# Kernel optimization log

Measured on AMD Instinct MI355X. Metric: run time of the kernel, lower is better.

Reference implementation:

```python
import jax, jax.numpy as jnp
import numpy as np

N = 100000
E = 1600000
C = 192      # in_channels
GH = 256     # grapher hidden
FH = 512     # ffn hidden
EPS = 1e-5


def _bn(x, gamma, beta):
    # BatchNorm1d, training-mode batch statistics over the node axis
    mean = jnp.mean(x, axis=0)
    var = jnp.var(x, axis=0)
    return (x - mean) * jax.lax.rsqrt(var + EPS) * gamma + beta


def setup_inputs() -> dict:
    key = jax.random.key(0)
    ks = jax.random.split(key, 12)
    s = 0.02
    inp = {
        "x": jax.random.normal(ks[0], (N, C), dtype=jnp.float32),
        "edge_index": jax.random.randint(ks[1], (2, E), 0, N, dtype=jnp.int64),
        # Grapher fc1
        "Wg1": jax.random.normal(ks[2], (C, GH), jnp.float32) * s,
        "bg1": jnp.zeros((GH,), jnp.float32),
        "gg1": jnp.ones((GH,), jnp.float32),
        "beg1": jnp.zeros((GH,), jnp.float32),
        # GraphConv (lin_rel has bias, lin_root no bias, per PyG)
        "Wrel": jax.random.normal(ks[3], (GH, GH), jnp.float32) * s,
        "brel": jnp.zeros((GH,), jnp.float32),
        "Wroot": jax.random.normal(ks[4], (GH, GH), jnp.float32) * s,
        # Grapher fc2
        "Wg2": jax.random.normal(ks[5], (GH, C), jnp.float32) * s,
        "bg2": jnp.zeros((C,), jnp.float32),
        "gg2": jnp.ones((C,), jnp.float32),
        "beg2": jnp.zeros((C,), jnp.float32),
        # FFN fc1
        "Wf1": jax.random.normal(ks[6], (C, FH), jnp.float32) * s,
        "bf1": jnp.zeros((FH,), jnp.float32),
        "gf1": jnp.ones((FH,), jnp.float32),
        "bef1": jnp.zeros((FH,), jnp.float32),
        # FFN fc2
        "Wf2": jax.random.normal(ks[7], (FH, C), jnp.float32) * s,
        "bf2": jnp.zeros((C,), jnp.float32),
        "gf2": jnp.ones((C,), jnp.float32),
        "bef2": jnp.zeros((C,), jnp.float32),
    }
    return inp


def reference(x, edge_index, Wg1, bg1, gg1, beg1, Wrel, brel, Wroot,
              Wg2, bg2, gg2, beg2, Wf1, bf1, gf1, bef1, Wf2, bf2, gf2, bef2):
    n = x.shape[0]
    src, dst = edge_index[0], edge_index[1]

    # ---- Grapher ----
    shortcut = x
    h = _bn(x @ Wg1 + bg1, gg1, beg1)                       # [N, GH]
    # GraphConv: sum-aggregate neighbor messages at target nodes
    agg = jax.ops.segment_sum(h[src], dst, num_segments=n)  # [N, GH]
    gc = agg @ Wrel + brel + h @ Wroot
    h = jax.nn.gelu(gc, approximate=False)
    h = _bn(h @ Wg2 + bg2, gg2, beg2)                       # [N, C]
    x = h + shortcut

    # ---- FFN ----
    shortcut = x
    h = jax.nn.gelu(_bn(x @ Wf1 + bf1, gf1, bef1), approximate=False)
    h = _bn(h @ Wf2 + bf2, gf2, bef2)
    return h + shortcut
```

## Files before the change

kernel.cpp:

```cpp
#include <hip/hip_runtime.h>
#include <math.h>

typedef __bf16 bf16x8 __attribute__((ext_vector_type(8)));
typedef float  floatx4 __attribute__((ext_vector_type(4)));

__device__ inline float bf_lo(unsigned u){ return __uint_as_float(u << 16); }
__device__ inline float bf_hi(unsigned u){ return __uint_as_float(u & 0xffff0000u); }
__device__ inline unsigned short f2bf_u(float f){
    unsigned u = __float_as_uint(f);
    return (unsigned short)((u + 0x7fffu + ((u >> 16) & 1u)) >> 16);
}
__device__ inline unsigned pack2(float a, float b){
    return (unsigned)f2bf_u(a) | ((unsigned)f2bf_u(b) << 16);
}
__device__ inline float gelu_f(float v){
    return 0.5f * v * (1.f + erff(v * 0.70710678118654752f));
}
__device__ inline void gload_lds16(const void* g, void* l){
    __builtin_amdgcn_global_load_lds(
        (const __attribute__((address_space(1))) unsigned int*)g,
        (__attribute__((address_space(3))) unsigned int*)l, 16, 0, 0);
}

__global__ void zero_k(int* __restrict__ p, int n){
    int i = blockIdx.x * 256 + threadIdx.x;
    if (i < n) p[i] = 0;
}

__global__ void xcast_k(const float* __restrict__ x, unsigned short* __restrict__ xb, long n8){
    long i = (long)blockIdx.x * 256 + threadIdx.x;
    if (i < n8){
        const float4* p = (const float4*)(x + i * 8);
        float4 a = p[0], b = p[1];
        uint4 o;
        o.x = pack2(a.x, a.y); o.y = pack2(a.z, a.w);
        o.z = pack2(b.x, b.y); o.w = pack2(b.z, b.w);
        *(uint4*)(xb + i * 8) = o;
    }
}

__global__ void wprep_k(const float* __restrict__ W, unsigned short* __restrict__ Wt,
                        int K, int Ncols, int ostride, int ooffs){
    int idx = blockIdx.x * 256 + threadIdx.x;
    if (idx < K * Ncols){
        int k = idx / Ncols, n = idx - k * Ncols;
        Wt[(size_t)n * ostride + ooffs + k] = f2bf_u(W[idx]);
    }
}


#define RBSH 9
#define RB   512
#define PCH  8192

__global__ __launch_bounds__(256)
void bhist_k(const int* __restrict__ dst, int* __restrict__ bcnt, int E){
    __shared__ int h[256];
    for (int i = threadIdx.x; i < 256; i += 256) h[i] = 0;
    __syncthreads();
    for (long i = (long)blockIdx.x * 256 + threadIdx.x; i < E; i += (long)gridDim.x * 256)
        atomicAdd(&h[dst[i] >> RBSH], 1);
    __syncthreads();
    int v = h[threadIdx.x];
    if (v) atomicAdd(&bcnt[threadIdx.x * 16], v);
}

__global__ void bscan_k(const int* __restrict__ bcnt, int* __restrict__ bbase,
                        int* __restrict__ bcur, int nbuk, int E){
    __shared__ int s[256];
    const int t = threadIdx.x;
    int v = (t < nbuk) ? bcnt[t * 16] : 0;
    s[t] = v; __syncthreads();
    for (int d = 1; d < 256; d <<= 1){
        int tt = (t >= d) ? s[t - d] : 0;
        __syncthreads();
        s[t] += tt;
        __syncthreads();
    }
    int excl = s[t] - v;
    if (t < nbuk){ bbase[t] = excl; bcur[t * 16] = excl; }
    if (t == 0) bbase[nbuk] = E;
}

__global__ __launch_bounds__(512)
void bpart_k(const int* __restrict__ src, const int* __restrict__ dst,
             int* __restrict__ bcur, int2* __restrict__ pairs, int E){
    __shared__ int h[256];
    __shared__ int s[256];
    __shared__ int cur[256];
    const int t = threadIdx.x;
    const int base = blockIdx.x * PCH;
    const int cnt = min(PCH, E - base);
    if (t < 256) h[t] = 0;
    __syncthreads();
    for (int i = t; i < cnt; i += 512)
        atomicAdd(&h[dst[base + i] >> RBSH], 1);
    __syncthreads();
    if (t < 256) s[t] = h[t];
    __syncthreads();
    for (int d = 1; d < 256; d <<= 1){
        int tt = 0;
        if (t < 256 && t >= d) tt = s[t - d];
        __syncthreads();
        if (t < 256) s[t] += tt;
        __syncthreads();
    }
    if (t < 256){
        int myc = h[t];
        int g = 0;
        if (myc) g = atomicAdd(&bcur[t * 16], myc);
        cur[t] = g;
    }
    __syncthreads();
    for (int i = t; i < cnt; i += 512){
        int d = dst[base + i];
        int b = d >> RBSH;
        int r = atomicAdd(&cur[b], 1);
        pairs[r] = make_int2(src[base + i], d);
    }
}

__global__ __launch_bounds__(1024)
void bbuild_k(const int2* __restrict__ pairs, const int* __restrict__ bbase,
              int* __restrict__ offsets, int* __restrict__ esrc, int N, int E){
    __shared__ int h[RB];
    __shared__ int s[RB];
    const int b = blockIdx.x;
    const int t = threadIdx.x;
    const int p0 = bbase[b], p1 = bbase[b + 1];
    if (t < RB) h[t] = 0;
    __syncthreads();
    for (int i = p0 + t; i < p1; i += 1024)
        atomicAdd(&h[pairs[i].y & (RB - 1)], 1);
    __syncthreads();
    int v = 0;
    if (t < RB){ v = h[t]; s[t] = v; }
    __syncthreads();
    for (int d = 1; d < RB; d <<= 1){
        int tt = 0;
        if (t < RB && t >= d) tt = s[t - d];
        __syncthreads();
        if (t < RB) s[t] += tt;
        __syncthreads();
    }
    if (t < RB){
        int node = (b << RBSH) + t;
        int excl = p0 + s[t] - v;
        if (node < N) offsets[node] = excl;
        h[t] = excl;
    }
    __syncthreads();
    for (int i = p0 + t; i < p1; i += 1024){
        int2 pr = pairs[i];
        int r = atomicAdd(&h[pr.y & (RB - 1)], 1);
        esrc[r] = pr.x;
    }
    if (b == 0 && t == 0) offsets[N] = E;
}

__global__ __launch_bounds__(256)
void agg_k(const unsigned short* __restrict__ hbn, const int* __restrict__ offsets,
           const int* __restrict__ esrc, unsigned short* __restrict__ aggout, int N){
    const int lane = threadIdx.x & 63;
    const int node = blockIdx.x * 4 + (threadIdx.x >> 6);
    if (node >= N) return;
    const int off  = offsets[node];
    const int end  = offsets[node + 1];
    const int half = lane >> 5;
    const int l32  = lane & 31;
    float a[8];
#pragma unroll
    for (int j = 0; j < 8; ++j) a[j] = 0.f;
    const unsigned short* hb = hbn + l32 * 8;
    for (int c = off; c < end; c += 64){
        const int e = c + lane;
        int sl = (e < end) ? esrc[e] : 0;
        const int cnt = min(64, end - c);
        for (int j = 0; j < cnt; j += 16){
            int   s[8];
            float m[8];
            uint4 u[8];
#pragma unroll
            for (int k = 0; k < 8; ++k){
                const int idx = j + 2 * k + half;
                s[k] = __shfl(sl, idx);
                m[k] = (idx < cnt) ? 1.f : 0.f;
            }
#pragma unroll
            for (int k = 0; k < 8; ++k)
                u[k] = *(const uint4*)(hb + (size_t)s[k] * 512);
#pragma unroll
            for (int k = 0; k < 8; ++k){
                a[0] = fmaf(m[k], bf_lo(u[k].x), a[0]);
                a[1] = fmaf(m[k], bf_hi(u[k].x), a[1]);
                a[2] = fmaf(m[k], bf_lo(u[k].y), a[2]);
                a[3] = fmaf(m[k], bf_hi(u[k].y), a[3]);
                a[4] = fmaf(m[k], bf_lo(u[k].z), a[4]);
                a[5] = fmaf(m[k], bf_hi(u[k].z), a[5]);
                a[6] = fmaf(m[k], bf_lo(u[k].w), a[6]);
                a[7] = fmaf(m[k], bf_hi(u[k].w), a[7]);
            }
        }
    }
#pragma unroll
    for (int j = 0; j < 8; ++j)
        a[j] += __shfl_xor(a[j], 32);
    if (half == 0){
        uint4 o;
        o.x = pack2(a[0], a[1]); o.y = pack2(a[2], a[3]);
        o.z = pack2(a[4], a[5]); o.w = pack2(a[6], a[7]);
        *(uint4*)(aggout + (size_t)node * 512 + l32 * 8) = o;
    }
}

template<int K, bool GELU_OUT>
__global__ __launch_bounds__(256)
void gemm3_k(const unsigned short* __restrict__ A, const unsigned short* __restrict__ Bt,
             const float* __restrict__ bias, unsigned short* __restrict__ Cp,
             long M, int NCOLS){
    __shared__ unsigned short Xs[128 * 64];
    __shared__ unsigned short Ws[64 * 64];
    const int t    = threadIdx.x;
    const int lane = t & 63;
    const int w    = t >> 6;
    const int r16  = lane & 15;
    const int q4   = lane >> 4;
    const long mbase = (long)blockIdx.x * 128;
    const int  cb    = blockIdx.y * 64;

    floatx4 acc[4][2];
#pragma unroll
    for (int ai = 0; ai < 4; ++ai)
#pragma unroll
        for (int bi = 0; bi < 2; ++bi) acc[ai][bi] = (floatx4)0.f;

    const int lrow = w * 8 + (lane >> 3);
    const int lk   = (lane & 7) * 8;
    const unsigned short* ga = A  + (size_t)(mbase + lrow) * K + lk;
    const unsigned short* gb = Bt + (size_t)(cb + lrow) * K + lk;
    unsigned short* lx = Xs + w * 512 + lane * 8;
    unsigned short* lw = Ws + w * 512 + lane * 8;

    for (int kt = 0; kt < K; kt += 64){
#pragma unroll
        for (int i = 0; i < 4; ++i)
            gload_lds16(ga + (size_t)i * 32 * K + kt, lx + i * 2048);
#pragma unroll
        for (int j = 0; j < 2; ++j)
            gload_lds16(gb + (size_t)j * 32 * K + kt, lw + j * 2048);
        asm volatile("s_waitcnt vmcnt(0)" ::: "memory");
        __syncthreads();
#pragma unroll
        for (int kc = 0; kc < 64; kc += 32){
            bf16x8 wf[4], xf[2];
#pragma unroll
            for (int ai = 0; ai < 4; ++ai)
                wf[ai] = *(const bf16x8*)(Ws + (ai * 16 + r16) * 64 + kc + q4 * 8);
#pragma unroll
            for (int bi = 0; bi < 2; ++bi)
                xf[bi] = *(const bf16x8*)(Xs + (w * 32 + bi * 16 + r16) * 64 + kc + q4 * 8);
#pragma unroll
            for (int ai = 0; ai < 4; ++ai)
#pragma unroll
                for (int bi = 0; bi < 2; ++bi)
                    acc[ai][bi] = __builtin_amdgcn_mfma_f32_16x16x32_bf16(
                        wf[ai], xf[bi], acc[ai][bi], 0, 0, 0);
        }
        __syncthreads();
    }

    float4 bv[4];
#pragma unroll
    for (int ai = 0; ai < 4; ++ai)
        bv[ai] = *(const float4*)(bias + cb + ai * 16 + q4 * 4);
#pragma unroll
    for (int bi = 0; bi < 2; ++bi){
        long node = mbase + w * 32 + bi * 16 + r16;
        if (node < M){
            unsigned short* cp = Cp + (size_t)node * NCOLS + cb;
#pragma unroll
            for (int ai = 0; ai < 4; ++ai){
                float v0 = acc[ai][bi][0] + bv[ai].x;
                float v1 = acc[ai][bi][1] + bv[ai].y;
                float v2 = acc[ai][bi][2] + bv[ai].z;
                float v3 = acc[ai][bi][3] + bv[ai].w;
                if constexpr (GELU_OUT){
                    v0 = gelu_f(v0); v1 = gelu_f(v1); v2 = gelu_f(v2); v3 = gelu_f(v3);
                }
                uint2 o; o.x = pack2(v0, v1); o.y = pack2(v2, v3);
                *(uint2*)(cp + ai * 16 + q4 * 4) = o;
            }
        }
    }
}

template<int NCOLS>
__global__ void colstats_k(const unsigned short* __restrict__ in,
                           float* __restrict__ gsum, float* __restrict__ gsq, long nrows){
    constexpr int TPR  = NCOLS / 8;
    constexpr int BDIM = (NCOLS == 192) ? 192 : 256;
    constexpr int ROWS = BDIM / TPR;
    __shared__ float sS[ROWS * NCOLS], sQ[ROWS * NCOLS];
    const int t  = threadIdx.x;
    const int c8 = (t % TPR) * 8;
    const int r  = t / TPR;
    float s[8], q[8];
#pragma unroll
    for (int j = 0; j < 8; ++j){ s[j] = 0.f; q[j] = 0.f; }
    for (long row = (long)blockIdx.x * ROWS + r; row < nrows; row += (long)gridDim.x * ROWS){
        uint4 u = *(const uint4*)(in + row * NCOLS + c8);
        float v[8];
        v[0] = bf_lo(u.x); v[1] = bf_hi(u.x); v[2] = bf_lo(u.y); v[3] = bf_hi(u.y);
        v[4] = bf_lo(u.z); v[5] = bf_hi(u.z); v[6] = bf_lo(u.w); v[7] = bf_hi(u.w);
#pragma unroll
        for (int j = 0; j < 8; ++j){ s[j] += v[j]; q[j] += v[j] * v[j]; }
    }
#pragma unroll
    for (int j = 0; j < 8; ++j){ sS[r * NCOLS + c8 + j] = s[j]; sQ[r * NCOLS + c8 + j] = q[j]; }
    __syncthreads();
    for (int c = t; c < NCOLS; c += BDIM){
        float as = 0.f, aq = 0.f;
#pragma unroll
        for (int rr = 0; rr < ROWS; ++rr){ as += sS[rr * NCOLS + c]; aq += sQ[rr * NCOLS + c]; }
        atomicAdd(&gsum[c], as);
        atomicAdd(&gsq[c],  aq);
    }
}

template<int NCOLS, bool GELU_OUT, bool RES, bool RES_F32, bool OUT_F32>
__global__ __launch_bounds__(256)
void bn_apply_k(const unsigned short* __restrict__ in, void* __restrict__ outv,
                const void* __restrict__ resv,
                const float* __restrict__ gsum, const float* __restrict__ gsq,
                const float* __restrict__ gamma, const float* __restrict__ beta,
                long nrows, int ostride, int ooffs, float invN){
    __shared__ float s_scale[NCOLS], s_shift[NCOLS];
    for (int c = threadIdx.x; c < NCOLS; c += 256){
        float mean = gsum[c] * invN;
        float var  = gsq[c] * invN - mean * mean;
        float sc   = gamma[c] * rsqrtf(var + 1e-5f);
        s_scale[c] = sc;
        s_shift[c] = beta[c] - mean * sc;
    }
    __syncthreads();
    long i8 = ((long)blockIdx.x * 256 + threadIdx.x) * 8;
    if (i8 >= nrows * (long)NCOLS) return;
    long row  = i8 / NCOLS;
    int  col0 = (int)(i8 - row * NCOLS);
    uint4 u = *(const uint4*)(in + i8);
    float v[8];
    v[0] = bf_lo(u.x); v[1] = bf_hi(u.x); v[2] = bf_lo(u.y); v[3] = bf_hi(u.y);
    v[4] = bf_lo(u.z); v[5] = bf_hi(u.z); v[6] = bf_lo(u.w); v[7] = bf_hi(u.w);
#pragma unroll
    for (int j = 0; j < 8; ++j){
        v[j] = v[j] * s_scale[col0 + j] + s_shift[col0 + j];
        if constexpr (GELU_OUT) v[j] = gelu_f(v[j]);
    }
    if constexpr (RES){
        if constexpr (RES_F32){
            const float4* rp = (const float4*)((const float*)resv + i8);
            float4 r0 = rp[0], r1 = rp[1];
            v[0] += r0.x; v[1] += r0.y; v[2] += r0.z; v[3] += r0.w;
            v[4] += r1.x; v[5] += r1.y; v[6] += r1.z; v[7] += r1.w;
        } else {
            uint4 r = *(const uint4*)((const unsigned short*)resv + i8);
            v[0] += bf_lo(r.x); v[1] += bf_hi(r.x); v[2] += bf_lo(r.y); v[3] += bf_hi(r.y);
            v[4] += bf_lo(r.z); v[5] += bf_hi(r.z); v[6] += bf_lo(r.w); v[7] += bf_hi(r.w);
        }
    }
    long opos = row * ostride + ooffs + col0;
    if constexpr (OUT_F32){
        float4* op = (float4*)((float*)outv + opos);
        op[0] = make_float4(v[0], v[1], v[2], v[3]);
        op[1] = make_float4(v[4], v[5], v[6], v[7]);
    } else {
        uint4 o;
        o.x = pack2(v[0], v[1]); o.y = pack2(v[2], v[3]);
        o.z = pack2(v[4], v[5]); o.w = pack2(v[6], v[7]);
        *(uint4*)((unsigned short*)outv + opos) = o;
    }
}

extern "C" void kernel_launch(void* const* d_in, const int* in_sizes, int n_in,
                              void* d_out, int out_size, void* d_ws, size_t ws_size,
                              hipStream_t stream){
    const int C = 192, GH = 256, FH = 512;
    const float* x    = (const float*)d_in[0];
    const int*   ei   = (const int*)d_in[1];
    const float* Wg1  = (const float*)d_in[2];
    const float* bg1  = (const float*)d_in[3];
    const float* gg1  = (const float*)d_in[4];
    const float* beg1 = (const float*)d_in[5];
    const float* Wrel = (const float*)d_in[6];
    const float* brel = (const float*)d_in[7];
    const float* Wroot= (const float*)d_in[8];
    const float* Wg2  = (const float*)d_in[9];
    const float* bg2  = (const float*)d_in[10];
    const float* gg2  = (const float*)d_in[11];
    const float* beg2 = (const float*)d_in[12];
    const float* Wf1  = (const float*)d_in[13];
    const float* bf1  = (const float*)d_in[14];
    const float* gf1  = (const float*)d_in[15];
    const float* bef1 = (const float*)d_in[16];
    const float* Wf2  = (const float*)d_in[17];
    const float* bf2  = (const float*)d_in[18];
    const float* gf2  = (const float*)d_in[19];
    const float* bef2 = (const float*)d_in[20];

    const int N = in_sizes[0] / C;
    const int E = in_sizes[1] / 2;
    const int* e_src = ei;
    const int* e_dst = ei + E;

    char* wp = (char*)d_ws;
    auto carve = [&](size_t bytes) -> void* {
        void* p = (void*)wp; wp += (bytes + 255) & ~(size_t)255; return p;
    };
    unsigned short* wt_g1 = (unsigned short*)carve((size_t)GH * C * 2);
    unsigned short* wt_rr = (unsigned short*)carve((size_t)GH * 512 * 2);
    unsigned short* wt_g2 = (unsigned short*)carve((size_t)C * GH * 2);
    unsigned short* wt_f1 = (unsigned short*)carve((size_t)FH * C * 2);
    unsigned short* wt_f2 = (unsigned short*)carve((size_t)C * FH * 2);
    float* stats = (float*)carve(2 * (size_t)(GH + C + FH + C) * 4);
    float* sum1 = stats;        float* sq1 = sum1 + GH;
    float* sum2 = sq1 + GH;     float* sq2 = sum2 + C;
    float* sum3 = sq2 + C;      float* sq3 = sum3 + FH;
    float* sum4 = sq3 + FH;     float* sq4 = sum4 + C;
    unsigned short* buf0  = (unsigned short*)carve((size_t)N * 512 * 2);
    unsigned short* bufAG = (unsigned short*)carve((size_t)N * 512 * 2);
    int* offsets = (int*)carve((size_t)(N + 1) * 4);
    int* esrc    = (int*)carve((size_t)E * 4);
    int* bcnt    = (int*)carve((size_t)256 * 16 * 4);
    int* bbase   = (int*)carve((size_t)257 * 4);
    int* bcur    = (int*)carve((size_t)256 * 16 * 4);
    unsigned short* x_bf = bufAG;
    int2* pairs = (int2*)buf0;
    unsigned short* h1  = buf0;
    unsigned short* g   = buf0;
    unsigned short* f1  = buf0;
    unsigned short* AG  = bufAG;
    unsigned short* h2  = bufAG;
    unsigned short* h4  = bufAG + (size_t)N * C;
    (void)ws_size; (void)n_in; (void)out_size;

    const float invN = 1.0f / (float)N;
    const int GB = (N + 127) / 128;
    const int nbuk = (N + RB - 1) >> RBSH;

    wprep_k<<<(C * GH + 255) / 256, 256, 0, stream>>>(Wg1, wt_g1, C, GH, C, 0);
    wprep_k<<<(GH * GH + 255) / 256, 256, 0, stream>>>(Wrel, wt_rr, GH, GH, 512, 0);
    wprep_k<<<(GH * GH + 255) / 256, 256, 0, stream>>>(Wroot, wt_rr, GH, GH, 512, GH);
    wprep_k<<<(GH * C + 255) / 256, 256, 0, stream>>>(Wg2, wt_g2, GH, C, GH, 0);
    wprep_k<<<(C * FH + 255) / 256, 256, 0, stream>>>(Wf1, wt_f1, C, FH, C, 0);
    wprep_k<<<(FH * C + 255) / 256, 256, 0, stream>>>(Wf2, wt_f2, FH, C, FH, 0);

    const int nstats = 2 * (GH + C + FH + C);
    zero_k<<<(nstats + 255) / 256, 256, 0, stream>>>((int*)stats, nstats);
    zero_k<<<(256 * 16 + 255) / 256, 256, 0, stream>>>(bcnt, 256 * 16);

    bhist_k<<<1024, 256, 0, stream>>>(e_dst, bcnt, E);
    bscan_k<<<1, 256, 0, stream>>>(bcnt, bbase, bcur, nbuk, E);
    bpart_k<<<(E + PCH - 1) / PCH, 512, 0, stream>>>(e_src, e_dst, bcur, pairs, E);
    bbuild_k<<<nbuk, 1024, 0, stream>>>(pairs, bbase, offsets, esrc, N, E);

    xcast_k<<<(int)(((size_t)N * C / 8 + 255) / 256), 256, 0, stream>>>(x, x_bf, (long)N * C / 8);

    gemm3_k<192, false><<<dim3(GB, GH / 64), 256, 0, stream>>>(x_bf, wt_g1, bg1, h1, N, GH);
    colstats_k<256><<<512, 256, 0, stream>>>(h1, sum1, sq1, N);
    bn_apply_k<256, false, false, false, false><<<(int)(((size_t)N * GH / 8 + 255) / 256), 256, 0, stream>>>(
        h1, AG, nullptr, sum1, sq1, gg1, beg1, N, 512, 256, invN);
    agg_k<<<(N + 3) / 4, 256, 0, stream>>>(AG + 256, offsets, esrc, AG, N);
    gemm3_k<512, true><<<dim3(GB, GH / 64), 256, 0, stream>>>(AG, wt_rr, brel, g, N, GH);
    gemm3_k<256, false><<<dim3(GB, C / 64), 256, 0, stream>>>(g, wt_g2, bg2, h2, N, C);
    colstats_k<192><<<512, 192, 0, stream>>>(h2, sum2, sq2, N);
    bn_apply_k<192, false, true, true, false><<<(int)(((size_t)N * C / 8 + 255) / 256), 256, 0, stream>>>(
        h2, h2, x, sum2, sq2, gg2, beg2, N, 192, 0, invN);

    gemm3_k<192, false><<<dim3(GB, FH / 64), 256, 0, stream>>>(h2, wt_f1, bf1, f1, N, FH);
    colstats_k<512><<<512, 256, 0, stream>>>(f1, sum3, sq3, N);
    bn_apply_k<512, true, false, false, false><<<(int)(((size_t)N * FH / 8 + 255) / 256), 256, 0, stream>>>(
        f1, f1, nullptr, sum3, sq3, gf1, bef1, N, 512, 0, invN);
    gemm3_k<512, false><<<dim3(GB, C / 64), 256, 0, stream>>>(f1, wt_f2, bf2, h4, N, C);
    colstats_k<192><<<512, 192, 0, stream>>>(h4, sum4, sq4, N);
    bn_apply_k<192, false, true, false, true><<<(int)(((size_t)N * C / 8 + 255) / 256), 256, 0, stream>>>(
        h4, d_out, h2, sum4, sq4, gf2, bef2, N, 192, 0, invN);
}
```

Baseline: 842.1 us.

## Fuse BN column stats into GEMM epilogues and fold first BN into GraphConv weights

Column sum and sum-of-squares are now accumulated in the GEMM epilogue with shuffle and LDS reduction plus atomics, which removes the four separate colstats passes that re-read each activation. The first BatchNorm is folded algebraically into the GraphConv. The pre-BN h1 goes straight into the aggregation buffer, the Wrel/Wroot weights are scaled by the BN scale, and the shift enters through a bias plus a per-node degree times rvec term computed from CSR offsets. This drops one full bn_apply pass over N×256. The cost is extra small kernels, aggregation over unnormalized values, and bf16 rounding of the scaled weights, which may change accuracy.

```diff
diff --git a/kernel.cpp b/kernel.cpp
--- a/kernel.cpp
+++ b/kernel.cpp
@@ -48,6 +48,40 @@
     }
 }
 
+__global__ void mkbn_k(const float* __restrict__ gsum, const float* __restrict__ gsq,
+                       const float* __restrict__ gamma, const float* __restrict__ beta,
+                       float* __restrict__ scv, float* __restrict__ shv, int C_, float invN){
+    int c = blockIdx.x * 256 + threadIdx.x;
+    if (c < C_){
+        float mean = gsum[c] * invN;
+        float var  = gsq[c] * invN - mean * mean;
+        float sc   = gamma[c] * rsqrtf(var + 1e-5f);
+        scv[c] = sc;
+        shv[c] = beta[c] - mean * sc;
+    }
+}
+
+__global__ void wscale_k(unsigned short* __restrict__ wt, const float* __restrict__ scv, int total){
+    int i = blockIdx.x * 256 + threadIdx.x;
+    if (i < total){
+        float v = __uint_as_float(((unsigned)wt[i]) << 16);
+        wt[i] = f2bf_u(v * scv[i & 255]);
+    }
+}
+
+__global__ void biasrr_k(const float* __restrict__ Wrel, const float* __restrict__ Wroot,
+                         const float* __restrict__ brel, const float* __restrict__ shv,
+                         float* __restrict__ bias2, float* __restrict__ rvec){
+    int m = threadIdx.x;
+    float b2 = 0.f, rv = 0.f;
+    for (int k = 0; k < 256; ++k){
+        float s = shv[k];
+        rv = fmaf(s, Wrel[k * 256 + m], rv);
+        b2 = fmaf(s, Wroot[k * 256 + m], b2);
+    }
+    bias2[m] = brel[m] + b2;
+    rvec[m]  = rv;
+}
 
 #define RBSH 9
 #define RB   512
@@ -213,11 +247,13 @@
     }
 }
 
-template<int K, bool GELU_OUT>
+template<int K, bool GELU_OUT, bool STATS, bool DEGBIAS>
 __global__ __launch_bounds__(256)
 void gemm3_k(const unsigned short* __restrict__ A, const unsigned short* __restrict__ Bt,
              const float* __restrict__ bias, unsigned short* __restrict__ Cp,
-             long M, int NCOLS){
+             long M, int ostride, int ooffs,
+             float* __restrict__ gsum, float* __restrict__ gsq,
+             const int* __restrict__ offs, const float* __restrict__ rvec){
     __shared__ unsigned short Xs[128 * 64];
     __shared__ unsigned short Ws[64 * 64];
     const int t    = threadIdx.x;
@@ -273,57 +309,90 @@
 #pragma unroll
     for (int ai = 0; ai < 4; ++ai)
         bv[ai] = *(const float4*)(bias + cb + ai * 16 + q4 * 4);
+    float4 rv[4];
+    if constexpr (DEGBIAS){
+#pragma unroll
+        for (int ai = 0; ai < 4; ++ai)
+            rv[ai] = *(const float4*)(rvec + cb + ai * 16 + q4 * 4);
+    }
+    float cs[4][4], cq[4][4];
+    if constexpr (STATS){
+#pragma unroll
+        for (int ai = 0; ai < 4; ++ai)
+#pragma unroll
+            for (int j = 0; j < 4; ++j){ cs[ai][j] = 0.f; cq[ai][j] = 0.f; }
+    }
 #pragma unroll
     for (int bi = 0; bi < 2; ++bi){
         long node = mbase + w * 32 + bi * 16 + r16;
-        if (node < M){
-            unsigned short* cp = Cp + (size_t)node * NCOLS + cb;
-#pragma unroll
-            for (int ai = 0; ai < 4; ++ai){
-                float v0 = acc[ai][bi][0] + bv[ai].x;
-                float v1 = acc[ai][bi][1] + bv[ai].y;
-                float v2 = acc[ai][bi][2] + bv[ai].z;
-                float v3 = acc[ai][bi][3] + bv[ai].w;
-                if constexpr (GELU_OUT){
-                    v0 = gelu_f(v0); v1 = gelu_f(v1); v2 = gelu_f(v2); v3 = gelu_f(v3);
+        const bool valid = node < M;
+        float degf = 0.f;
+        if constexpr (DEGBIAS){
+            if (valid) degf = (float)(offs[node + 1] - offs[node]);
+        }
+        unsigned short* cp = Cp + (size_t)node * ostride + ooffs + cb;
+#pragma unroll
+        for (int ai = 0; ai < 4; ++ai){
+            float v[4];
+            v[0] = acc[ai][bi][0] + bv[ai].x;
+            v[1] = acc[ai][bi][1] + bv[ai].y;
+            v[2] = acc[ai][bi][2] + bv[ai].z;
+            v[3] = acc[ai][bi][3] + bv[ai].w;
+            if constexpr (DEGBIAS){
+                v[0] = fmaf(degf, rv[ai].x, v[0]);
+                v[1] = fmaf(degf, rv[ai].y, v[1]);
+                v[2] = fmaf(degf, rv[ai].z, v[2]);
+                v[3] = fmaf(degf, rv[ai].w, v[3]);
+            }
+            if constexpr (STATS){
+#pragma unroll
+                for (int j = 0; j < 4; ++j){
+                    float vv = valid ? v[j] : 0.f;
+                    cs[ai][j] += vv;
+                    cq[ai][j] = fmaf(vv, vv, cq[ai][j]);
                 }
-                uint2 o; o.x = pack2(v0, v1); o.y = pack2(v2, v3);
+            }
+            if constexpr (GELU_OUT){
+                v[0] = gelu_f(v[0]); v[1] = gelu_f(v[1]);
+                v[2] = gelu_f(v[2]); v[3] = gelu_f(v[3]);
+            }
+            if (valid){
+                uint2 o; o.x = pack2(v[0], v[1]); o.y = pack2(v[2], v[3]);
                 *(uint2*)(cp + ai * 16 + q4 * 4) = o;
             }
         }
     }
-}
-
-template<int NCOLS>
-__global__ void colstats_k(const unsigned short* __restrict__ in,
-                           float* __restrict__ gsum, float* __restrict__ gsq, long nrows){
-    constexpr int TPR  = NCOLS / 8;
-    constexpr int BDIM = (NCOLS == 192) ? 192 : 256;
-    constexpr int ROWS = BDIM / TPR;
-    __shared__ float sS[ROWS * NCOLS], sQ[ROWS * NCOLS];
-    const int t  = threadIdx.x;
-    const int c8 = (t % TPR) * 8;
-    const int r  = t / TPR;
-    float s[8], q[8];
-#pragma unroll
-    for (int j = 0; j < 8; ++j){ s[j] = 0.f; q[j] = 0.f; }
-    for (long row = (long)blockIdx.x * ROWS + r; row < nrows; row += (long)gridDim.x * ROWS){
-        uint4 u = *(const uint4*)(in + row * NCOLS + c8);
-        float v[8];
-        v[0] = bf_lo(u.x); v[1] = bf_hi(u.x); v[2] = bf_lo(u.y); v[3] = bf_hi(u.y);
-        v[4] = bf_lo(u.z); v[5] = bf_hi(u.z); v[6] = bf_lo(u.w); v[7] = bf_hi(u.w);
-#pragma unroll
-        for (int j = 0; j < 8; ++j){ s[j] += v[j]; q[j] += v[j] * v[j]; }
-    }
-#pragma unroll
-    for (int j = 0; j < 8; ++j){ sS[r * NCOLS + c8 + j] = s[j]; sQ[r * NCOLS + c8 + j] = q[j]; }
-    __syncthreads();
-    for (int c = t; c < NCOLS; c += BDIM){
-        float as = 0.f, aq = 0.f;
-#pragma unroll
-        for (int rr = 0; rr < ROWS; ++rr){ as += sS[rr * NCOLS + c]; aq += sQ[rr * NCOLS + c]; }
-        atomicAdd(&gsum[c], as);
-        atomicAdd(&gsq[c],  aq);
+
+    if constexpr (STATS){
+#pragma unroll
+        for (int ai = 0; ai < 4; ++ai)
+#pragma unroll
+            for (int j = 0; j < 4; ++j){
+#pragma unroll
+                for (int m = 1; m < 16; m <<= 1){
+                    cs[ai][j] += __shfl_xor(cs[ai][j], m);
+                    cq[ai][j] += __shfl_xor(cq[ai][j], m);
+                }
+            }
+        float* ssum = (float*)Xs;
+        float* ssq  = ssum + 256;
+        if (r16 == 0){
+#pragma unroll
+            for (int ai = 0; ai < 4; ++ai)
+#pragma unroll
+                for (int j = 0; j < 4; ++j){
+                    ssum[w * 64 + ai * 16 + q4 * 4 + j] = cs[ai][j];
+                    ssq [w * 64 + ai * 16 + q4 * 4 + j] = cq[ai][j];
+                }
+        }
+        __syncthreads();
+        if (t < 64){
+            float s = 0.f, q = 0.f;
+#pragma unroll
+            for (int ww = 0; ww < 4; ++ww){ s += ssum[ww * 64 + t]; q += ssq[ww * 64 + t]; }
+            atomicAdd(&gsum[cb + t], s);
+            atomicAdd(&gsq [cb + t], q);
+        }
     }
 }
 
@@ -426,6 +495,10 @@
     float* sum2 = sq1 + GH;     float* sq2 = sum2 + C;
     float* sum3 = sq2 + C;      float* sq3 = sum3 + FH;
     float* sum4 = sq3 + FH;     float* sq4 = sum4 + C;
+    float* scv   = (float*)carve(256 * 4);
+    float* shv   = (float*)carve(256 * 4);
+    float* bias2 = (float*)carve(256 * 4);
+    float* rvec  = (float*)carve(256 * 4);
     unsigned short* buf0  = (unsigned short*)carve((size_t)N * 512 * 2);
     unsigned short* bufAG = (unsigned short*)carve((size_t)N * 512 * 2);
     int* offsets = (int*)carve((size_t)(N + 1) * 4);
@@ -433,14 +506,13 @@
     int* bcnt    = (int*)carve((size_t)256 * 16 * 4);
     int* bbase   = (int*)carve((size_t)257 * 4);
     int* bcur    = (int*)carve((size_t)256 * 16 * 4);
-    unsigned short* x_bf = bufAG;
     int2* pairs = (int2*)buf0;
-    unsigned short* h1  = buf0;
-    unsigned short* g   = buf0;
-    unsigned short* f1  = buf0;
-    unsigned short* AG  = bufAG;
-    unsigned short* h2  = bufAG;
-    unsigned short* h4  = bufAG + (size_t)N * C;
+    unsigned short* x_bf = buf0;
+    unsigned short* g    = buf0;
+    unsigned short* f1   = buf0;
+    unsigned short* AG   = bufAG;
+    unsigned short* h2   = bufAG;
+    unsigned short* h4   = bufAG + (size_t)N * C;
     (void)ws_size; (void)n_in; (void)out_size;
 
     const float invN = 1.0f / (float)N;
@@ -465,23 +537,25 @@
 
     xcast_k<<<(int)(((size_t)N * C / 8 + 255) / 256), 256, 0, stream>>>(x, x_bf, (long)N * C / 8);
 
-    gemm3_k<192, false><<<dim3(GB, GH / 64), 256, 0, stream>>>(x_bf, wt_g1, bg1, h1, N, GH);
-    colstats_k<256><<<512, 256, 0, stream>>>(h1, sum1, sq1, N);
-    bn_apply_k<256, false, false, false, false><<<(int)(((size_t)N * GH / 8 + 255) / 256), 256, 0, stream>>>(
-        h1, AG, nullptr, sum1, sq1, gg1, beg1, N, 512, 256, invN);
+    gemm3_k<192, false, true, false><<<dim3(GB, GH / 64), 256, 0, stream>>>(
+        x_bf, wt_g1, bg1, AG, N, 512, 256, sum1, sq1, nullptr, nullptr);
+    mkbn_k<<<1, 256, 0, stream>>>(sum1, sq1, gg1, beg1, scv, shv, GH, invN);
+    wscale_k<<<(GH * 512 + 255) / 256, 256, 0, stream>>>(wt_rr, scv, GH * 512);
+    biasrr_k<<<1, 256, 0, stream>>>(Wrel, Wroot, brel, shv, bias2, rvec);
     agg_k<<<(N + 3) / 4, 256, 0, stream>>>(AG + 256, offsets, esrc, AG, N);
-    gemm3_k<512, true><<<dim3(GB, GH / 64), 256, 0, stream>>>(AG, wt_rr, brel, g, N, GH);
-    gemm3_k<256, false><<<dim3(GB, C / 64), 256, 0, stream>>>(g, wt_g2, bg2, h2, N, C);
-    colstats_k<192><<<512, 192, 0, stream>>>(h2, sum2, sq2, N);
+    gemm3_k<512, true, false, true><<<dim3(GB, GH / 64), 256, 0, stream>>>(
+        AG, wt_rr, bias2, g, N, GH, 0, nullptr, nullptr, offsets, rvec);
+    gemm3_k<256, false, true, false><<<dim3(GB, C / 64), 256, 0, stream>>>(
+        g, wt_g2, bg2, h2, N, C, 0, sum2, sq2, nullptr, nullptr);
     bn_apply_k<192, false, true, true, false><<<(int)(((size_t)N * C / 8 + 255) / 256), 256, 0, stream>>>(
         h2, h2, x, sum2, sq2, gg2, beg2, N, 192, 0, invN);
 
-    gemm3_k<192, false><<<dim3(GB, FH / 64), 256, 0, stream>>>(h2, wt_f1, bf1, f1, N, FH);
-    colstats_k<512><<<512, 256, 0, stream>>>(f1, sum3, sq3, N);
+    gemm3_k<192, false, true, false><<<dim3(GB, FH / 64), 256, 0, stream>>>(
+        h2, wt_f1, bf1, f1, N, FH, 0, sum3, sq3, nullptr, nullptr);
     bn_apply_k<512, true, false, false, false><<<(int)(((size_t)N * FH / 8 + 255) / 256), 256, 0, stream>>>(
         f1, f1, nullptr, sum3, sq3, gf1, bef1, N, 512, 0, invN);
-    gemm3_k<512, false><<<dim3(GB, C / 64), 256, 0, stream>>>(f1, wt_f2, bf2, h4, N, C);
-    colstats_k<192><<<512, 192, 0, stream>>>(h4, sum4, sq4, N);
+    gemm3_k<512, false, true, false><<<dim3(GB, C / 64), 256, 0, stream>>>(
+        f1, wt_f2, bf2, h4, N, C, 0, sum4, sq4, nullptr, nullptr);
     bn_apply_k<192, false, true, false, true><<<(int)(((size_t)N * C / 8 + 255) / 256), 256, 0, stream>>>(
         h4, d_out, h2, sum4, sq4, gf2, bef2, N, 192, 0, invN);
 }
```

After: 903.1 us. 1.07x slower.

## Fold first BatchNorm into GraphConv weights and remap GEMM blocks per XCD

Applied to the files above, without the earlier changes.

The first BatchNorm apply pass is removed. The raw fc1 output is written straight into the aggregation buffer, and the BN scale is folded into the combined Wrel/Wroot weights. The BN shift becomes a per-column bias term, plus a degree-weighted correction (deg * shift·Wrel) added in the GraphConv GEMM epilogue. GEMM launches move to a 1D grid whose block IDs are remapped so that consecutive tiles share an XCD, aiming at better L2 locality. In exchange it adds several tiny kernels, and aggregating un-normalized bf16 values can shift rounding behaviour.

```diff
diff --git a/kernel.cpp b/kernel.cpp
--- a/kernel.cpp
+++ b/kernel.cpp
@@ -48,6 +48,46 @@
     }
 }
 
+__global__ void mkbn_k(const float* __restrict__ gsum, const float* __restrict__ gsq,
+                       const float* __restrict__ gamma, const float* __restrict__ beta,
+                       const float* __restrict__ brel,
+                       float* __restrict__ scv, float* __restrict__ shv,
+                       float* __restrict__ bias2, float* __restrict__ rvec,
+                       int C_, float invN){
+    int c = blockIdx.x * 256 + threadIdx.x;
+    if (c < C_){
+        float mean = gsum[c] * invN;
+        float var  = gsq[c] * invN - mean * mean;
+        float sc   = gamma[c] * rsqrtf(var + 1e-5f);
+        scv[c] = sc;
+        shv[c] = beta[c] - mean * sc;
+        bias2[c] = brel[c];
+        rvec[c]  = 0.f;
+    }
+}
+
+__global__ void wscale_k(unsigned short* __restrict__ wt, const float* __restrict__ scv, int total){
+    int i = blockIdx.x * 256 + threadIdx.x;
+    if (i < total){
+        float v = __uint_as_float(((unsigned)wt[i]) << 16);
+        wt[i] = f2bf_u(v * scv[i & 255]);
+    }
+}
+
+__global__ void biasrr_k(const float* __restrict__ Wrel, const float* __restrict__ Wroot,
+                         const float* __restrict__ shv,
+                         float* __restrict__ bias2, float* __restrict__ rvec){
+    int m = threadIdx.x;
+    int k0 = blockIdx.x * 32;
+    float b2 = 0.f, rv = 0.f;
+    for (int k = k0; k < k0 + 32; ++k){
+        float s = shv[k];
+        rv = fmaf(s, Wrel[k * 256 + m], rv);
+        b2 = fmaf(s, Wroot[k * 256 + m], b2);
+    }
+    atomicAdd(&bias2[m], b2);
+    atomicAdd(&rvec[m],  rv);
+}
 
 #define RBSH 9
 #define RB   512
@@ -213,11 +253,12 @@
     }
 }
 
-template<int K, bool GELU_OUT>
+template<int K, bool GELU_OUT, bool DEGBIAS>
 __global__ __launch_bounds__(256)
 void gemm3_k(const unsigned short* __restrict__ A, const unsigned short* __restrict__ Bt,
              const float* __restrict__ bias, unsigned short* __restrict__ Cp,
-             long M, int NCOLS){
+             long M, int NY, int ostride, int ooffs,
+             const int* __restrict__ offs, const float* __restrict__ rvec){
     __shared__ unsigned short Xs[128 * 64];
     __shared__ unsigned short Ws[64 * 64];
     const int t    = threadIdx.x;
@@ -225,8 +266,16 @@
     const int w    = t >> 6;
     const int r16  = lane & 15;
     const int q4   = lane >> 4;
-    const long mbase = (long)blockIdx.x * 128;
-    const int  cb    = blockIdx.y * 64;
+
+    const int nwg  = gridDim.x;
+    const int orig = blockIdx.x;
+    const int qq   = nwg >> 3, rr = nwg & 7;
+    const int xcd  = orig & 7, kk = orig >> 3;
+    const int wgid = (xcd < rr ? xcd * (qq + 1) : rr * (qq + 1) + (xcd - rr) * qq) + kk;
+    const int xb   = wgid / NY;
+    const int yb   = wgid - xb * NY;
+    const long mbase = (long)xb * 128;
+    const int  cb    = yb * 64;
 
     floatx4 acc[4][2];
 #pragma unroll
@@ -273,17 +322,31 @@
 #pragma unroll
     for (int ai = 0; ai < 4; ++ai)
         bv[ai] = *(const float4*)(bias + cb + ai * 16 + q4 * 4);
+    float4 rv[4];
+    if constexpr (DEGBIAS){
+#pragma unroll
+        for (int ai = 0; ai < 4; ++ai)
+            rv[ai] = *(const float4*)(rvec + cb + ai * 16 + q4 * 4);
+    }
 #pragma unroll
     for (int bi = 0; bi < 2; ++bi){
         long node = mbase + w * 32 + bi * 16 + r16;
         if (node < M){
-            unsigned short* cp = Cp + (size_t)node * NCOLS + cb;
+            float degf = 0.f;
+            if constexpr (DEGBIAS) degf = (float)(offs[node + 1] - offs[node]);
+            unsigned short* cp = Cp + (size_t)node * ostride + ooffs + cb;
 #pragma unroll
             for (int ai = 0; ai < 4; ++ai){
                 float v0 = acc[ai][bi][0] + bv[ai].x;
                 float v1 = acc[ai][bi][1] + bv[ai].y;
                 float v2 = acc[ai][bi][2] + bv[ai].z;
                 float v3 = acc[ai][bi][3] + bv[ai].w;
+                if constexpr (DEGBIAS){
+                    v0 = fmaf(degf, rv[ai].x, v0);
+                    v1 = fmaf(degf, rv[ai].y, v1);
+                    v2 = fmaf(degf, rv[ai].z, v2);
+                    v3 = fmaf(degf, rv[ai].w, v3);
+                }
                 if constexpr (GELU_OUT){
                     v0 = gelu_f(v0); v1 = gelu_f(v1); v2 = gelu_f(v2); v3 = gelu_f(v3);
                 }
@@ -296,7 +359,8 @@
 
 template<int NCOLS>
 __global__ void colstats_k(const unsigned short* __restrict__ in,
-                           float* __restrict__ gsum, float* __restrict__ gsq, long nrows){
+                           float* __restrict__ gsum, float* __restrict__ gsq,
+                           long nrows, int ostride, int ooffs){
     constexpr int TPR  = NCOLS / 8;
     constexpr int BDIM = (NCOLS == 192) ? 192 : 256;
     constexpr int ROWS = BDIM / TPR;
@@ -308,7 +372,7 @@
 #pragma unroll
     for (int j = 0; j < 8; ++j){ s[j] = 0.f; q[j] = 0.f; }
     for (long row = (long)blockIdx.x * ROWS + r; row < nrows; row += (long)gridDim.x * ROWS){
-        uint4 u = *(const uint4*)(in + row * NCOLS + c8);
+        uint4 u = *(const uint4*)(in + row * ostride + ooffs + c8);
         float v[8];
         v[0] = bf_lo(u.x); v[1] = bf_hi(u.x); v[2] = bf_lo(u.y); v[3] = bf_hi(u.y);
         v[4] = bf_lo(u.z); v[5] = bf_hi(u.z); v[6] = bf_lo(u.w); v[7] = bf_hi(u.w);
@@ -426,6 +490,10 @@
     float* sum2 = sq1 + GH;     float* sq2 = sum2 + C;
     float* sum3 = sq2 + C;      float* sq3 = sum3 + FH;
     float* sum4 = sq3 + FH;     float* sq4 = sum4 + C;
+    float* scv   = (float*)carve(256 * 4);
+    float* shv   = (float*)carve(256 * 4);
+    float* bias2 = (float*)carve(256 * 4);
+    float* rvec  = (float*)carve(256 * 4);
     unsigned short* buf0  = (unsigned short*)carve((size_t)N * 512 * 2);
     unsigned short* bufAG = (unsigned short*)carve((size_t)N * 512 * 2);
     int* offsets = (int*)carve((size_t)(N + 1) * 4);
@@ -433,14 +501,13 @@
     int* bcnt    = (int*)carve((size_t)256 * 16 * 4);
     int* bbase   = (int*)carve((size_t)257 * 4);
     int* bcur    = (int*)carve((size_t)256 * 16 * 4);
-    unsigned short* x_bf = bufAG;
     int2* pairs = (int2*)buf0;
-    unsigned short* h1  = buf0;
-    unsigned short* g   = buf0;
-    unsigned short* f1  = buf0;
-    unsigned short* AG  = bufAG;
-    unsigned short* h2  = bufAG;
-    unsigned short* h4  = bufAG + (size_t)N * C;
+    unsigned short* x_bf = buf0;
+    unsigned short* g    = buf0;
+    unsigned short* f1   = buf0;
+    unsigned short* AG   = bufAG;
+    unsigned short* h2   = bufAG;
+    unsigned short* h4   = bufAG + (size_t)N * C;
     (void)ws_size; (void)n_in; (void)out_size;
 
     const float invN = 1.0f / (float)N;
@@ -465,23 +532,29 @@
 
     xcast_k<<<(int)(((size_t)N * C / 8 + 255) / 256), 256, 0, stream>>>(x, x_bf, (long)N * C / 8);
 
-    gemm3_k<192, false><<<dim3(GB, GH / 64), 256, 0, stream>>>(x_bf, wt_g1, bg1, h1, N, GH);
-    colstats_k<256><<<512, 256, 0, stream>>>(h1, sum1, sq1, N);
-    bn_apply_k<256, false, false, false, false><<<(int)(((size_t)N * GH / 8 + 255) / 256), 256, 0, stream>>>(
-        h1, AG, nullptr, sum1, sq1, gg1, beg1, N, 512, 256, invN);
+    gemm3_k<192, false, false><<<GB * (GH / 64), 256, 0, stream>>>(
+        x_bf, wt_g1, bg1, AG, N, GH / 64, 512, 256, nullptr, nullptr);
+    colstats_k<256><<<512, 256, 0, stream>>>(AG, sum1, sq1, N, 512, 256);
+    mkbn_k<<<1, 256, 0, stream>>>(sum1, sq1, gg1, beg1, brel, scv, shv, bias2, rvec, GH, invN);
+    wscale_k<<<(GH * 512 + 255) / 256, 256, 0, stream>>>(wt_rr, scv, GH * 512);
+    biasrr_k<<<8, 256, 0, stream>>>(Wrel, Wroot, shv, bias2, rvec);
     agg_k<<<(N + 3) / 4, 256, 0, stream>>>(AG + 256, offsets, esrc, AG, N);
-    gemm3_k<512, true><<<dim3(GB, GH / 64), 256, 0, stream>>>(AG, wt_rr, brel, g, N, GH);
-    gemm3_k<256, false><<<dim3(GB, C / 64), 256, 0, stream>>>(g, wt_g2, bg2, h2, N, C);
-    colstats_k<192><<<512, 192, 0, stream>>>(h2, sum2, sq2, N);
+    gemm3_k<512, true, true><<<GB * (GH / 64), 256, 0, stream>>>(
+        AG, wt_rr, bias2, g, N, GH / 64, GH, 0, offsets, rvec);
+    gemm3_k<256, false, false><<<GB * (C / 64), 256, 0, stream>>>(
+        g, wt_g2, bg2, h2, N, C / 64, C, 0, nullptr, nullptr);
+    colstats_k<192><<<512, 192, 0, stream>>>(h2, sum2, sq2, N, 192, 0);
     bn_apply_k<192, false, true, true, false><<<(int)(((size_t)N * C / 8 + 255) / 256), 256, 0, stream>>>(
         h2, h2, x, sum2, sq2, gg2, beg2, N, 192, 0, invN);
 
-    gemm3_k<192, false><<<dim3(GB, FH / 64), 256, 0, stream>>>(h2, wt_f1, bf1, f1, N, FH);
-    colstats_k<512><<<512, 256, 0, stream>>>(f1, sum3, sq3, N);
+    gemm3_k<192, false, false><<<GB * (FH / 64), 256, 0, stream>>>(
+        h2, wt_f1, bf1, f1, N, FH / 64, FH, 0, nullptr, nullptr);
+    colstats_k<512><<<512, 256, 0, stream>>>(f1, sum3, sq3, N, 512, 0);
     bn_apply_k<512, true, false, false, false><<<(int)(((size_t)N * FH / 8 + 255) / 256), 256, 0, stream>>>(
         f1, f1, nullptr, sum3, sq3, gf1, bef1, N, 512, 0, invN);
-    gemm3_k<512, false><<<dim3(GB, C / 64), 256, 0, stream>>>(f1, wt_f2, bf2, h4, N, C);
-    colstats_k<192><<<512, 192, 0, stream>>>(h4, sum4, sq4, N);
+    gemm3_k<512, false, false><<<GB * (C / 64), 256, 0, stream>>>(
+        f1, wt_f2, bf2, h4, N, C / 64, C, 0, nullptr, nullptr);
+    colstats_k<192><<<512, 192, 0, stream>>>(h4, sum4, sq4, N, 192, 0);
     bn_apply_k<192, false, true, false, true><<<(int)(((size_t)N * C / 8 + 255) / 256), 256, 0, stream>>>(
         h4, d_out, h2, sum4, sq4, gf2, bef2, N, 192, 0, invN);
 }
```

Result: faster. 778.0 us (-7.6%).
